# Kernel optimization log

Hardware: AMD Instinct MI355X
Metric: run time of the kernel (lower is better)

Reference implementation:

```python
import jax, jax.numpy as jnp
import numpy as np

IGNORE_INDEX = 255
NUM_CLASSES = 19


def setup_inputs() -> dict:
    key = jax.random.key(0)
    k1, k2 = jax.random.split(key)
    logits = jax.random.normal(k1, (8, NUM_CLASSES, 512, 1024), dtype=jnp.float32)
    labels = jax.random.randint(k2, (8, 512, 1024), 0, NUM_CLASSES, dtype=jnp.int64)
    return {"logits": logits, "labels": labels}


def _lovasz_per_class(err, fg, valid):
    # err, fg, valid: [N] for one class. Sort by error descending.
    order = jnp.argsort(-err)
    es = err[order]
    fs = fg[order]
    vs = valid[order]
    gts = fs.sum()
    intersection = gts - jnp.cumsum(fs)
    # invalid (ignored) pixels contribute to neither fg nor background: vs - fs
    union = gts + jnp.cumsum(vs - fs)
    safe_union = jnp.where(union == 0, 1.0, union)
    jaccard = 1.0 - intersection / safe_union
    grad = jnp.concatenate([jaccard[:1], jaccard[1:] - jaccard[:-1]])
    loss_c = jnp.dot(es, grad)
    present = (gts > 0).astype(es.dtype)
    return loss_c, present


def reference(logits, labels):
    B, C, H, W = logits.shape
    probs = jax.nn.softmax(logits, axis=1)
    probs = probs.transpose(0, 2, 3, 1).reshape(-1, C)  # [N, C]
    lab = labels.reshape(-1)
    valid = (lab != IGNORE_INDEX).astype(probs.dtype)  # [N]
    # one-hot foreground per class, zeroed at ignored pixels
    fg = (lab[:, None] == jnp.arange(C)[None, :]).astype(probs.dtype) * valid[:, None]
    # errors; ignored pixels get error 0 so they sort to the end and contribute 0
    errors = jnp.abs(fg - probs) * valid[:, None]  # [N, C]
    loss_c, present = jax.vmap(_lovasz_per_class, in_axes=(1, 1, None))(errors, fg, valid)
    n_present = jnp.maximum(present.sum(), 1.0)
    return jnp.sum(loss_c * present) / n_present
```

## Files before the change

### kernel.cpp

```cpp
#include <hip/hip_runtime.h>


#define NCLS 19
#define IGNORE_IDX 255

constexpr int HW = 512 * 1024;
constexpr int HW4 = HW / 4;
constexpr int NQUAD = 8 * HW4;
constexpr int NBINS = 256;
constexpr int HSLOTS = NCLS * NBINS;
constexpr int PSTRIDE = HSLOTS + 1;
constexpr int NCOPY = 4;

__device__ __forceinline__ float fast_rcp(float x) {
#if defined(__has_builtin) && __has_builtin(__builtin_amdgcn_rcpf)
    return __builtin_amdgcn_rcpf(x);
#else
    return 1.0f / x;
#endif
}

template <int NHB>
__global__ __launch_bounds__(256) void lovasz_hist(
    const float* __restrict__ logits,
    const int*   __restrict__ labels,
    unsigned int* __restrict__ partial)
{
    constexpr int QPB = NQUAD / NHB;
    constexpr int QPT = QPB / 256;
    __shared__ unsigned int lh[NCOPY * PSTRIDE];
    const int t = threadIdx.x;
    for (int i = t; i < NCOPY * PSTRIDE; i += 256) lh[i] = 0;
    __syncthreads();

    unsigned int* my = lh + (t & (NCOPY - 1)) * PSTRIDE;

    for (int k = 0; k < QPT; ++k) {
        const int q   = blockIdx.x * QPB + k * 256 + t;
        const int b   = q >> 17;
        const int hw4 = q & (HW4 - 1);
        const float* base = logits + (size_t)b * NCLS * HW + (size_t)hw4 * 4;

        float ex[NCLS], ey[NCLS], ez[NCLS], ew[NCLS];
        float dx = 0.f, dy = 0.f, dz = 0.f, dw = 0.f;
#pragma unroll
        for (int c = 0; c < NCLS; ++c) {
            const float4 l = *(const float4*)(base + (size_t)c * HW);
            ex[c] = __expf(l.x); dx += ex[c];
            ey[c] = __expf(l.y); dy += ey[c];
            ez[c] = __expf(l.z); dz += ez[c];
            ew[c] = __expf(l.w); dw += ew[c];
        }
        const float rx = (float)NBINS * fast_rcp(dx);
        const float ry = (float)NBINS * fast_rcp(dy);
        const float rz = (float)NBINS * fast_rcp(dz);
        const float rw = (float)NBINS * fast_rcp(dw);

        const int4 lab = *(const int4*)(labels + (size_t)q * 4);

        auto upd = [&](int c, float psc, int lb) {
            if (lb == IGNORE_IDX) return;
            const bool fg = (lb == c);
            const float bs = fg ? ((float)NBINS - psc) : psc;
            int bin = (int)bs;
            bin = bin > NBINS - 1 ? NBINS - 1 : bin;
            atomicAdd(&my[c * NBINS + bin], fg ? 0x10001u : 1u);
        };
#pragma unroll
        for (int c = 0; c < NCLS; ++c) {
            upd(c, ex[c] * rx, lab.x);
            upd(c, ey[c] * ry, lab.y);
            upd(c, ez[c] * rz, lab.z);
            upd(c, ew[c] * rw, lab.w);
        }
    }
    __syncthreads();
    unsigned int* dst = partial + (size_t)blockIdx.x * HSLOTS;
    for (int i = t; i < HSLOTS; i += 256)
        dst[i] = lh[i] + lh[i + PSTRIDE] + lh[i + 2 * PSTRIDE] + lh[i + 3 * PSTRIDE];
}

__global__ __launch_bounds__(256) void lovasz_scan(
    const unsigned int* __restrict__ partial,
    int nhb,
    float* __restrict__ lp)
{
    const int c = blockIdx.x;
    const int t = threadIdx.x;

    unsigned int v = 0, g = 0;
    {
        const unsigned int* p0 = partial + c * NBINS + (NBINS - 1 - t);
        int b = 0;
        for (; b + 4 <= nhb; b += 4) {
            const unsigned int x0 = p0[(size_t)(b + 0) * HSLOTS];
            const unsigned int x1 = p0[(size_t)(b + 1) * HSLOTS];
            const unsigned int x2 = p0[(size_t)(b + 2) * HSLOTS];
            const unsigned int x3 = p0[(size_t)(b + 3) * HSLOTS];
            v += (x0 & 0xFFFFu) + (x1 & 0xFFFFu) + (x2 & 0xFFFFu) + (x3 & 0xFFFFu);
            g += (x0 >> 16) + (x1 >> 16) + (x2 >> 16) + (x3 >> 16);
        }
        for (; b < nhb; ++b) {
            const unsigned int x = p0[(size_t)b * HSLOTS];
            v += x & 0xFFFFu; g += x >> 16;
        }
    }

    __shared__ unsigned int pg[257], pv[257];
    pg[t + 1] = g; pv[t + 1] = v;
    __syncthreads();
    if (t == 0) {
        pg[0] = 0; pv[0] = 0;
        for (int i = 1; i <= 256; ++i) { pg[i] += pg[i - 1]; pv[i] += pv[i - 1]; }
    }
    __syncthreads();
    const unsigned int G = pg[256];

    double acc = 0.0;
    if (G > 0 && v) {
        const unsigned int CF = pg[t], CV = pv[t];
        const int bin = NBINS - 1 - t;
        const float e  = ((float)bin + 0.5f) * (1.0f / (float)NBINS);
        const float U0 = (float)(G - CF + CV);
        if (g) acc += (double)(e * (float)g / U0);
        const unsigned int nbg = v - g;
        if (nbg) {
            const float I1 = (float)(G - CF - g);
            acc += (double)(e * I1 * (float)nbg / (U0 * (U0 + (float)nbg)));
        }
    }

    __shared__ double sacc[256];
    sacc[t] = acc;
    __syncthreads();
    for (int s = 128; s > 0; s >>= 1) {
        if (t < s) sacc[t] += sacc[t + s];
        __syncthreads();
    }
    if (t == 0) {
        lp[c] = (float)sacc[0];
        lp[NCLS + c] = (G > 0) ? 1.0f : 0.0f;
    }
}

__global__ void lovasz_final(const float* __restrict__ lp, float* __restrict__ out) {
    if (threadIdx.x == 0) {
        float s = 0.f, np = 0.f;
        for (int c = 0; c < NCLS; ++c) { s += lp[c] * lp[NCLS + c]; np += lp[NCLS + c]; }
        out[0] = s / fmaxf(np, 1.0f);
    }
}

extern "C" void kernel_launch(void* const* d_in, const int* in_sizes, int n_in,
                              void* d_out, int out_size, void* d_ws, size_t ws_size,
                              hipStream_t stream) {
    const float* logits = (const float*)d_in[0];
    const int*   labels = (const int*)d_in[1];
    float* out = (float*)d_out;

    unsigned int* partial = (unsigned int*)d_ws;
    const size_t need512 = (size_t)512 * HSLOTS * sizeof(unsigned int) + 64 * sizeof(float);

    if (ws_size >= need512) {
        float* lp = (float*)(partial + (size_t)512 * HSLOTS);
        lovasz_hist<512><<<512, 256, 0, stream>>>(logits, labels, partial);
        lovasz_scan<<<NCLS, 256, 0, stream>>>(partial, 512, lp);
        lovasz_final<<<1, 64, 0, stream>>>(lp, out);
    } else {
        float* lp = (float*)(partial + (size_t)256 * HSLOTS);
        lovasz_hist<256><<<256, 256, 0, stream>>>(logits, labels, partial);
        lovasz_scan<<<NCLS, 256, 0, stream>>>(partial, 256, lp);
        lovasz_final<<<1, 64, 0, stream>>>(lp, out);
    }
}
```

Baseline: 469.0 us.

## Widen scan to 1024 threads and fold final reduction via last-block atomic

The scan kernel now uses 1024 threads per class, with four chunks each reducing a quarter of the partial histograms, and the chunks are then combined in shared memory. The separate final kernel is removed. The last scan block to finish, detected with an atomic counter that the hist kernel resets, computes the output. This cuts serial read latency in the scan and saves one kernel launch, at the cost of a fence and an atomic.

Measured after the change: 450.3 us. 4.0% less time.

```diff
diff --git a/kernel.cpp b/kernel.cpp
--- a/kernel.cpp
+++ b/kernel.cpp
@@ -24,12 +24,14 @@
 __global__ __launch_bounds__(256) void lovasz_hist(
     const float* __restrict__ logits,
     const int*   __restrict__ labels,
-    unsigned int* __restrict__ partial)
+    unsigned int* __restrict__ partial,
+    unsigned int* __restrict__ done)
 {
     constexpr int QPB = NQUAD / NHB;
     constexpr int QPT = QPB / 256;
     __shared__ unsigned int lh[NCOPY * PSTRIDE];
     const int t = threadIdx.x;
+    if (blockIdx.x == 0 && t == 0) *done = 0;
     for (int i = t; i < NCOPY * PSTRIDE; i += 256) lh[i] = 0;
     __syncthreads();
 
@@ -80,36 +82,52 @@
         dst[i] = lh[i] + lh[i + PSTRIDE] + lh[i + 2 * PSTRIDE] + lh[i + 3 * PSTRIDE];
 }
 
-__global__ __launch_bounds__(256) void lovasz_scan(
+template <int NHB>
+__global__ __launch_bounds__(1024) void lovasz_scan(
     const unsigned int* __restrict__ partial,
-    int nhb,
-    float* __restrict__ lp)
+    float* __restrict__ lp,
+    unsigned int* __restrict__ done,
+    float* __restrict__ out)
 {
+    constexpr int NPER = NHB / 4;
     const int c = blockIdx.x;
-    const int t = threadIdx.x;
+    const int j = threadIdx.x & 255;
+    const int chunk = threadIdx.x >> 8;
 
     unsigned int v = 0, g = 0;
     {
-        const unsigned int* p0 = partial + c * NBINS + (NBINS - 1 - t);
-        int b = 0;
-        for (; b + 4 <= nhb; b += 4) {
-            const unsigned int x0 = p0[(size_t)(b + 0) * HSLOTS];
-            const unsigned int x1 = p0[(size_t)(b + 1) * HSLOTS];
-            const unsigned int x2 = p0[(size_t)(b + 2) * HSLOTS];
-            const unsigned int x3 = p0[(size_t)(b + 3) * HSLOTS];
-            v += (x0 & 0xFFFFu) + (x1 & 0xFFFFu) + (x2 & 0xFFFFu) + (x3 & 0xFFFFu);
-            g += (x0 >> 16) + (x1 >> 16) + (x2 >> 16) + (x3 >> 16);
-        }
-        for (; b < nhb; ++b) {
-            const unsigned int x = p0[(size_t)b * HSLOTS];
-            v += x & 0xFFFFu; g += x >> 16;
+        const unsigned int* p0 = partial + c * NBINS + (NBINS - 1 - j)
+                               + (size_t)chunk * NPER * HSLOTS;
+#pragma unroll 1
+        for (int b = 0; b < NPER; b += 8) {
+            unsigned int x0 = p0[(size_t)(b + 0) * HSLOTS];
+            unsigned int x1 = p0[(size_t)(b + 1) * HSLOTS];
+            unsigned int x2 = p0[(size_t)(b + 2) * HSLOTS];
+            unsigned int x3 = p0[(size_t)(b + 3) * HSLOTS];
+            unsigned int x4 = p0[(size_t)(b + 4) * HSLOTS];
+            unsigned int x5 = p0[(size_t)(b + 5) * HSLOTS];
+            unsigned int x6 = p0[(size_t)(b + 6) * HSLOTS];
+            unsigned int x7 = p0[(size_t)(b + 7) * HSLOTS];
+            v += (x0 & 0xFFFFu) + (x1 & 0xFFFFu) + (x2 & 0xFFFFu) + (x3 & 0xFFFFu)
+               + (x4 & 0xFFFFu) + (x5 & 0xFFFFu) + (x6 & 0xFFFFu) + (x7 & 0xFFFFu);
+            g += (x0 >> 16) + (x1 >> 16) + (x2 >> 16) + (x3 >> 16)
+               + (x4 >> 16) + (x5 >> 16) + (x6 >> 16) + (x7 >> 16);
         }
     }
 
+    __shared__ unsigned int sv[1024], sg[1024];
+    sv[threadIdx.x] = v; sg[threadIdx.x] = g;
+    __syncthreads();
+
     __shared__ unsigned int pg[257], pv[257];
-    pg[t + 1] = g; pv[t + 1] = v;
+    unsigned int vv = 0, gg = 0;
+    if (threadIdx.x < 256) {
+        vv = sv[j] + sv[256 + j] + sv[512 + j] + sv[768 + j];
+        gg = sg[j] + sg[256 + j] + sg[512 + j] + sg[768 + j];
+        pg[j + 1] = gg; pv[j + 1] = vv;
+    }
     __syncthreads();
-    if (t == 0) {
+    if (threadIdx.x == 0) {
         pg[0] = 0; pv[0] = 0;
         for (int i = 1; i <= 256; ++i) { pg[i] += pg[i - 1]; pv[i] += pv[i - 1]; }
     }
@@ -117,36 +135,39 @@
     const unsigned int G = pg[256];
 
     double acc = 0.0;
-    if (G > 0 && v) {
-        const unsigned int CF = pg[t], CV = pv[t];
-        const int bin = NBINS - 1 - t;
+    if (threadIdx.x < 256 && G > 0 && vv) {
+        const unsigned int CF = pg[j], CV = pv[j];
+        const int bin = NBINS - 1 - j;
         const float e  = ((float)bin + 0.5f) * (1.0f / (float)NBINS);
         const float U0 = (float)(G - CF + CV);
-        if (g) acc += (double)(e * (float)g / U0);
-        const unsigned int nbg = v - g;
+        if (gg) acc += (double)(e * (float)gg / U0);
+        const unsigned int nbg = vv - gg;
         if (nbg) {
-            const float I1 = (float)(G - CF - g);
+            const float I1 = (float)(G - CF - gg);
             acc += (double)(e * I1 * (float)nbg / (U0 * (U0 + (float)nbg)));
         }
     }
 
     __shared__ double sacc[256];
-    sacc[t] = acc;
+    if (threadIdx.x < 256) sacc[threadIdx.x] = acc;
     __syncthreads();
     for (int s = 128; s > 0; s >>= 1) {
-        if (t < s) sacc[t] += sacc[t + s];
+        if (threadIdx.x < s) sacc[threadIdx.x] += sacc[threadIdx.x + s];
         __syncthreads();
     }
-    if (t == 0) {
+
+    __shared__ int is_last;
+    if (threadIdx.x == 0) {
         lp[c] = (float)sacc[0];
         lp[NCLS + c] = (G > 0) ? 1.0f : 0.0f;
+        __threadfence();
+        is_last = (atomicAdd(done, 1u) == NCLS - 1);
     }
-}
-
-__global__ void lovasz_final(const float* __restrict__ lp, float* __restrict__ out) {
-    if (threadIdx.x == 0) {
+    __syncthreads();
+    if (is_last && threadIdx.x == 0) {
+        __threadfence();
         float s = 0.f, np = 0.f;
-        for (int c = 0; c < NCLS; ++c) { s += lp[c] * lp[NCLS + c]; np += lp[NCLS + c]; }
+        for (int i = 0; i < NCLS; ++i) { s += lp[i] * lp[NCLS + i]; np += lp[NCLS + i]; }
         out[0] = s / fmaxf(np, 1.0f);
     }
 }
@@ -159,17 +180,17 @@
     float* out = (float*)d_out;
 
     unsigned int* partial = (unsigned int*)d_ws;
-    const size_t need512 = (size_t)512 * HSLOTS * sizeof(unsigned int) + 64 * sizeof(float);
+    const size_t need512 = ((size_t)512 * HSLOTS + 80) * sizeof(unsigned int);
 
     if (ws_size >= need512) {
         float* lp = (float*)(partial + (size_t)512 * HSLOTS);
-        lovasz_hist<512><<<512, 256, 0, stream>>>(logits, labels, partial);
-        lovasz_scan<<<NCLS, 256, 0, stream>>>(partial, 512, lp);
-        lovasz_final<<<1, 64, 0, stream>>>(lp, out);
+        unsigned int* done = (unsigned int*)(lp + 64);
+        lovasz_hist<512><<<512, 256, 0, stream>>>(logits, labels, partial, done);
+        lovasz_scan<512><<<NCLS, 1024, 0, stream>>>(partial, lp, done, out);
     } else {
         float* lp = (float*)(partial + (size_t)256 * HSLOTS);
-        lovasz_hist<256><<<256, 256, 0, stream>>>(logits, labels, partial);
-        lovasz_scan<<<NCLS, 256, 0, stream>>>(partial, 256, lp);
-        lovasz_final<<<1, 64, 0, stream>>>(lp, out);
+        unsigned int* done = (unsigned int*)(lp + 64);
+        lovasz_hist<256><<<256, 256, 0, stream>>>(logits, labels, partial, done);
+        lovasz_scan<256><<<NCLS, 1024, 0, stream>>>(partial, lp, done, out);
     }
 }
```
